# Optimization experiments

Measured on AMD Instinct MI355X. Metric: run time of the kernel, lower is better.

Reference implementation:

```python
import jax, jax.numpy as jnp
import numpy as np

MARGIN = 0.5


def _pairwise_sq_dists(x):
    # [N, N] squared euclidean distances
    sq = jnp.sum(x * x, axis=-1)  # [N]
    d = sq[:, None] + sq[None, :] - 2.0 * (x @ x.T)
    return jnp.maximum(d, 0.0)


def setup_inputs() -> dict:
    key = jax.random.key(0)
    k1, k2 = jax.random.split(key)
    N, D, NUM_CLASSES = 8192, 64, 128
    embeddings = jax.random.normal(k1, (N, D), dtype=jnp.float32)
    targets = jax.random.randint(k2, (N,), 0, NUM_CLASSES, dtype=jnp.int64)
    return {"embeddings": embeddings, "targets": targets}


def reference(embeddings, targets):
    # Batch-hard online triplet mining (vectorized form of the CPU loop):
    # for each anchor i: hard positive = argmax dist over same-class,
    # hard negative = argmin dist over other-class.
    dist = _pairwise_sq_dists(embeddings)  # [N, N]
    same = targets[:, None] == targets[None, :]  # [N, N] bool
    hard_pos = jnp.argmax(jnp.where(same, dist, -jnp.inf), axis=1)  # [N]
    hard_neg = jnp.argmin(jnp.where(same, jnp.inf, dist), axis=1)  # [N]
    # Recompute squared distances from embeddings for the selected triplets
    ap = jnp.sum(jnp.square(embeddings - embeddings[hard_pos]), axis=1)  # [N]
    an = jnp.sum(jnp.square(embeddings - embeddings[hard_neg]), axis=1)  # [N]
    losses = jax.nn.relu(ap - an + MARGIN)
    return jnp.mean(losses)
```

## Files before the change

### kernel.cpp

```cpp
#include <hip/hip_runtime.h>
#include <stdint.h>

#define N 8192
#define Dq 64
#define SPLITS 12
#define MARGIN 0.5f

typedef __attribute__((ext_vector_type(8))) short short8;
typedef __attribute__((ext_vector_type(16))) float floatx16;

__device__ __forceinline__ unsigned short f2bf(float f) {
  unsigned u = __float_as_uint(f);
  u += 0x7FFF + ((u >> 16) & 1);
  return (unsigned short)(u >> 16);
}

__global__ __launch_bounds__(256) void prep_kernel(
    const float* __restrict__ emb,
    unsigned short* __restrict__ embB, float* __restrict__ sq,
    float* __restrict__ out) {
  int tid = blockIdx.x * 256 + threadIdx.x;
  int row = tid >> 4;
  int c = tid & 15;
  float4 v = reinterpret_cast<const float4*>(emb)[row * 16 + c];
  float s = v.x * v.x + v.y * v.y + v.z * v.z + v.w * v.w;
  #pragma unroll
  for (int off = 1; off < 16; off <<= 1) s += __shfl_xor(s, off);
  if (c == 0) sq[row] = s;
  ushort4 b;
  b.x = f2bf(v.x); b.y = f2bf(v.y); b.z = f2bf(v.z); b.w = f2bf(v.w);
  reinterpret_cast<ushort4*>(embB)[row * 16 + c] = b;
  if (tid == 0) out[0] = 0.f;
}

__global__ __launch_bounds__(256, 3) void mine_kernel(
    const unsigned short* __restrict__ embB,
    const float* __restrict__ sq, const int* __restrict__ cls,
    unsigned* __restrict__ pmax, unsigned* __restrict__ pmin) {
  const int lane = threadIdx.x & 63;
  const int wave = threadIdx.x >> 6;
  const int lo = lane & 31;
  const int half = lane >> 5;
  const int rowBase = (blockIdx.x * 4 + wave) * 32;
  const int split = blockIdx.y;
  const int t0 = (256 * split) / SPLITS;
  const int t1 = (256 * (split + 1)) / SPLITS;

  const short8* ea =
      reinterpret_cast<const short8*>(embB + (size_t)(rowBase + lo) * Dq + half * 8);
  short8 a0 = ea[0], a1 = ea[2], a2 = ea[4], a3 = ea[6];

  float sqi[16]; int ci[16];
  #pragma unroll
  for (int r = 0; r < 16; ++r) {
    int row = rowBase + (r & 3) + 8 * (r >> 2) + 4 * half;
    sqi[r] = sq[row]; ci[r] = cls[row];
  }

  unsigned maxk[16], mink[16];
  #pragma unroll
  for (int r = 0; r < 16; ++r) { maxk[r] = 0u; mink[r] = 0xFFFFFFFFu; }

  for (int t = t0; t < t1; ++t) {
    const int cb = t * 32;
    const short8* eb =
        reinterpret_cast<const short8*>(embB + (size_t)(cb + lo) * Dq + half * 8);
    short8 b0 = eb[0], b1 = eb[2], b2 = eb[4], b3 = eb[6];
    float sqj = sq[cb + lo];
    int cj = cls[cb + lo];

    floatx16 acc;
    #pragma unroll
    for (int i = 0; i < 16; ++i) acc[i] = 0.f;
    acc = __builtin_amdgcn_mfma_f32_32x32x16_bf16(a0, b0, acc, 0, 0, 0);
    acc = __builtin_amdgcn_mfma_f32_32x32x16_bf16(a1, b1, acc, 0, 0, 0);
    acc = __builtin_amdgcn_mfma_f32_32x32x16_bf16(a2, b2, acc, 0, 0, 0);
    acc = __builtin_amdgcn_mfma_f32_32x32x16_bf16(a3, b3, acc, 0, 0, 0);

    const unsigned j = cb + lo;
    const unsigned jinv = 8191u - j;
    #pragma unroll
    for (int r = 0; r < 16; ++r) {
      float d = fmaf(acc[r], -2.0f, sqi[r]) + sqj;
      d = fmaxf(d, 0.0f);
      unsigned kb = __float_as_uint(d) & 0xFFFFE000u;
      bool same = (ci[r] == cj);
      unsigned kp = same ? (kb | jinv) : 0u;
      unsigned kn = same ? 0xFFFFFFFFu : (kb | j);
      maxk[r] = maxk[r] > kp ? maxk[r] : kp;
      mink[r] = mink[r] < kn ? mink[r] : kn;
    }
  }

  #pragma unroll
  for (int off = 1; off < 32; off <<= 1) {
    #pragma unroll
    for (int r = 0; r < 16; ++r) {
      unsigned om = (unsigned)__shfl_xor((int)maxk[r], off);
      maxk[r] = maxk[r] > om ? maxk[r] : om;
      unsigned on = (unsigned)__shfl_xor((int)mink[r], off);
      mink[r] = mink[r] < on ? mink[r] : on;
    }
  }

  if (lo == 0) {
    #pragma unroll
    for (int r = 0; r < 16; ++r) {
      int row = rowBase + (r & 3) + 8 * (r >> 2) + 4 * half;
      pmax[split * N + row] = maxk[r];
      pmin[split * N + row] = mink[r];
    }
  }
}

__global__ __launch_bounds__(256) void finalize_kernel(
    const float* __restrict__ emb,
    const unsigned* __restrict__ pmax, const unsigned* __restrict__ pmin,
    float* __restrict__ out) {
  int tid = blockIdx.x * 256 + threadIdx.x;
  int anchor = tid >> 2;
  int part = tid & 3;
  unsigned Kp = 0u, Kn = 0xFFFFFFFFu;
  #pragma unroll
  for (int s = 0; s < SPLITS; ++s) {
    unsigned vp = pmax[s * N + anchor];
    Kp = Kp > vp ? Kp : vp;
    unsigned vn = pmin[s * N + anchor];
    Kn = Kn < vn ? Kn : vn;
  }
  int jp = 8191 - (int)(Kp & 8191u);
  int jn = (int)(Kn & 8191u);

  const float4* xi = reinterpret_cast<const float4*>(emb + (size_t)anchor * Dq) + part * 4;
  const float4* xp = reinterpret_cast<const float4*>(emb + (size_t)jp * Dq) + part * 4;
  const float4* xn = reinterpret_cast<const float4*>(emb + (size_t)jn * Dq) + part * 4;
  float ap = 0.f, an = 0.f;
  #pragma unroll
  for (int k = 0; k < 4; ++k) {
    float4 a = xi[k], p = xp[k], q = xn[k];
    float dx = a.x - p.x, dy = a.y - p.y, dz = a.z - p.z, dw = a.w - p.w;
    ap += dx * dx + dy * dy + dz * dz + dw * dw;
    dx = a.x - q.x; dy = a.y - q.y; dz = a.z - q.z; dw = a.w - q.w;
    an += dx * dx + dy * dy + dz * dz + dw * dw;
  }
  #pragma unroll
  for (int off = 1; off < 4; off <<= 1) {
    ap += __shfl_xor(ap, off);
    an += __shfl_xor(an, off);
  }
  float loss = (part == 0) ? fmaxf(ap - an + MARGIN, 0.f) : 0.f;
  #pragma unroll
  for (int off = 4; off < 64; off <<= 1) loss += __shfl_xor(loss, off);
  __shared__ float wsum[4];
  if ((threadIdx.x & 63) == 0) wsum[threadIdx.x >> 6] = loss;
  __syncthreads();
  if (threadIdx.x == 0)
    atomicAdd(out, (wsum[0] + wsum[1] + wsum[2] + wsum[3]) * (1.0f / (float)N));
}

extern "C" void kernel_launch(void* const* d_in, const int* in_sizes, int n_in,
                              void* d_out, int out_size, void* d_ws, size_t ws_size,
                              hipStream_t stream) {
  const float* emb = (const float*)d_in[0];
  const int* tgt = (const int*)d_in[1];
  float* out = (float*)d_out;

  char* ws = (char*)d_ws;
  unsigned short* embB = (unsigned short*)ws;
  float* sq = (float*)(ws + (size_t)N * Dq * 2);
  char* p = ws + (size_t)N * Dq * 2 + (size_t)N * 4;
  unsigned* pmax = (unsigned*)p; p += (size_t)SPLITS * N * 4;
  unsigned* pmin = (unsigned*)p;

  prep_kernel<<<N * 16 / 256, 256, 0, stream>>>(emb, embB, sq, out);
  mine_kernel<<<dim3(N / 128, SPLITS), 256, 0, stream>>>(embB, sq, tgt, pmax, pmin);
  finalize_kernel<<<N * 4 / 256, 256, 0, stream>>>(emb, pmax, pmin, out);
}
```

Before: 100.4 us.

## Fold squared-norm terms into an extra MFMA and merge splits with atomics

Squared norms are stored as bf16 values pre-scaled to -(0.5*s+2) and folded into a fifth MFMA via augmented A/B vectors, so the accumulator directly yields a monotone surrogate of the distance. This removes the per-element fma/add/max epilogue. Per-split partial buffers are replaced by atomicMax/atomicMin into a single array initialized in prep, which removes the finalize reduction loop. Splits go from 12 to 16, occupancy is raised to 4 and the loop is unrolled by 2. The changes add an extra MFMA per tile and bf16 rounding of the norms, and they drop the clamp at zero, which may change argmin/argmax ties.

```diff
diff --git a/kernel.cpp b/kernel.cpp
--- a/kernel.cpp
+++ b/kernel.cpp
@@ -3,7 +3,7 @@
 
 #define N 8192
 #define Dq 64
-#define SPLITS 12
+#define SPLITS 16
 #define MARGIN 0.5f
 
 typedef __attribute__((ext_vector_type(8))) short short8;
@@ -17,7 +17,8 @@
 
 __global__ __launch_bounds__(256) void prep_kernel(
     const float* __restrict__ emb,
-    unsigned short* __restrict__ embB, float* __restrict__ sq,
+    unsigned short* __restrict__ embB, unsigned short* __restrict__ sqb,
+    unsigned* __restrict__ pmax, unsigned* __restrict__ pmin,
     float* __restrict__ out) {
   int tid = blockIdx.x * 256 + threadIdx.x;
   int row = tid >> 4;
@@ -26,48 +27,52 @@
   float s = v.x * v.x + v.y * v.y + v.z * v.z + v.w * v.w;
   #pragma unroll
   for (int off = 1; off < 16; off <<= 1) s += __shfl_xor(s, off);
-  if (c == 0) sq[row] = s;
+  if (c == 0) sqb[row] = f2bf(-(0.5f * s + 2.0f));
   ushort4 b;
   b.x = f2bf(v.x); b.y = f2bf(v.y); b.z = f2bf(v.z); b.w = f2bf(v.w);
   reinterpret_cast<ushort4*>(embB)[row * 16 + c] = b;
+  if (tid < N) { pmax[tid] = 0u; pmin[tid] = 0xFFFFFFFFu; }
   if (tid == 0) out[0] = 0.f;
 }
 
-__global__ __launch_bounds__(256, 3) void mine_kernel(
+__global__ __launch_bounds__(256, 4) void mine_kernel(
     const unsigned short* __restrict__ embB,
-    const float* __restrict__ sq, const int* __restrict__ cls,
+    const unsigned short* __restrict__ sqb, const int* __restrict__ cls,
     unsigned* __restrict__ pmax, unsigned* __restrict__ pmin) {
   const int lane = threadIdx.x & 63;
   const int wave = threadIdx.x >> 6;
   const int lo = lane & 31;
   const int half = lane >> 5;
   const int rowBase = (blockIdx.x * 4 + wave) * 32;
-  const int split = blockIdx.y;
-  const int t0 = (256 * split) / SPLITS;
-  const int t1 = (256 * (split + 1)) / SPLITS;
+  const int tBase = blockIdx.y * (256 / SPLITS);
 
   const short8* ea =
       reinterpret_cast<const short8*>(embB + (size_t)(rowBase + lo) * Dq + half * 8);
   short8 a0 = ea[0], a1 = ea[2], a2 = ea[4], a3 = ea[6];
+  unsigned short sqm = sqb[rowBase + lo];
+  const short one = (short)0x3F80;
+  short8 a4 = {(short)(half == 0 ? one : 0),
+               (short)(half == 0 ? (short)sqm : 0), 0, 0, 0, 0, 0, 0};
 
-  float sqi[16]; int ci[16];
+  int ci[16];
   #pragma unroll
-  for (int r = 0; r < 16; ++r) {
-    int row = rowBase + (r & 3) + 8 * (r >> 2) + 4 * half;
-    sqi[r] = sq[row]; ci[r] = cls[row];
-  }
+  for (int r = 0; r < 16; ++r)
+    ci[r] = cls[rowBase + (r & 3) + 8 * (r >> 2) + 4 * half];
 
   unsigned maxk[16], mink[16];
   #pragma unroll
   for (int r = 0; r < 16; ++r) { maxk[r] = 0u; mink[r] = 0xFFFFFFFFu; }
 
-  for (int t = t0; t < t1; ++t) {
-    const int cb = t * 32;
+  #pragma unroll 2
+  for (int t = 0; t < 256 / SPLITS; ++t) {
+    const int cb = (tBase + t) * 32;
     const short8* eb =
         reinterpret_cast<const short8*>(embB + (size_t)(cb + lo) * Dq + half * 8);
     short8 b0 = eb[0], b1 = eb[2], b2 = eb[4], b3 = eb[6];
-    float sqj = sq[cb + lo];
+    unsigned short sqn = sqb[cb + lo];
     int cj = cls[cb + lo];
+    short8 b4 = {(short)(half == 0 ? (short)sqn : 0),
+                 (short)(half == 0 ? one : 0), 0, 0, 0, 0, 0, 0};
 
     floatx16 acc;
     #pragma unroll
@@ -76,14 +81,13 @@
     acc = __builtin_amdgcn_mfma_f32_32x32x16_bf16(a1, b1, acc, 0, 0, 0);
     acc = __builtin_amdgcn_mfma_f32_32x32x16_bf16(a2, b2, acc, 0, 0, 0);
     acc = __builtin_amdgcn_mfma_f32_32x32x16_bf16(a3, b3, acc, 0, 0, 0);
+    acc = __builtin_amdgcn_mfma_f32_32x32x16_bf16(a4, b4, acc, 0, 0, 0);
 
     const unsigned j = cb + lo;
     const unsigned jinv = 8191u - j;
     #pragma unroll
     for (int r = 0; r < 16; ++r) {
-      float d = fmaf(acc[r], -2.0f, sqi[r]) + sqj;
-      d = fmaxf(d, 0.0f);
-      unsigned kb = __float_as_uint(d) & 0xFFFFE000u;
+      unsigned kb = __float_as_uint(acc[r]) & 0xFFFFE000u;
       bool same = (ci[r] == cj);
       unsigned kp = same ? (kb | jinv) : 0u;
       unsigned kn = same ? 0xFFFFFFFFu : (kb | j);
@@ -107,8 +111,8 @@
     #pragma unroll
     for (int r = 0; r < 16; ++r) {
       int row = rowBase + (r & 3) + 8 * (r >> 2) + 4 * half;
-      pmax[split * N + row] = maxk[r];
-      pmin[split * N + row] = mink[r];
+      atomicMax(&pmax[row], maxk[r]);
+      atomicMin(&pmin[row], mink[r]);
     }
   }
 }
@@ -120,16 +124,8 @@
   int tid = blockIdx.x * 256 + threadIdx.x;
   int anchor = tid >> 2;
   int part = tid & 3;
-  unsigned Kp = 0u, Kn = 0xFFFFFFFFu;
-  #pragma unroll
-  for (int s = 0; s < SPLITS; ++s) {
-    unsigned vp = pmax[s * N + anchor];
-    Kp = Kp > vp ? Kp : vp;
-    unsigned vn = pmin[s * N + anchor];
-    Kn = Kn < vn ? Kn : vn;
-  }
-  int jp = 8191 - (int)(Kp & 8191u);
-  int jn = (int)(Kn & 8191u);
+  int jp = 8191 - (int)(pmax[anchor] & 8191u);
+  int jn = (int)(pmin[anchor] & 8191u);
 
   const float4* xi = reinterpret_cast<const float4*>(emb + (size_t)anchor * Dq) + part * 4;
   const float4* xp = reinterpret_cast<const float4*>(emb + (size_t)jp * Dq) + part * 4;
@@ -167,12 +163,11 @@
 
   char* ws = (char*)d_ws;
   unsigned short* embB = (unsigned short*)ws;
-  float* sq = (float*)(ws + (size_t)N * Dq * 2);
-  char* p = ws + (size_t)N * Dq * 2 + (size_t)N * 4;
-  unsigned* pmax = (unsigned*)p; p += (size_t)SPLITS * N * 4;
-  unsigned* pmin = (unsigned*)p;
+  unsigned short* sqb = (unsigned short*)(ws + (size_t)N * Dq * 2);
+  unsigned* pmax = (unsigned*)(ws + (size_t)N * Dq * 2 + N * 2);
+  unsigned* pmin = pmax + N;
 
-  prep_kernel<<<N * 16 / 256, 256, 0, stream>>>(emb, embB, sq, out);
-  mine_kernel<<<dim3(N / 128, SPLITS), 256, 0, stream>>>(embB, sq, tgt, pmax, pmin);
+  prep_kernel<<<N * 16 / 256, 256, 0, stream>>>(emb, embB, sqb, pmax, pmin, out);
+  mine_kernel<<<dim3(N / 128, SPLITS), 256, 0, stream>>>(embB, sqb, tgt, pmax, pmin);
   finalize_kernel<<<N * 4 / 256, 256, 0, stream>>>(emb, pmax, pmin, out);
 }
```

Measured after the change: 99.63 us. About the same (-0.8%).
